# Kernel optimization log

Hardware: AMD Instinct MI355X
Metric: run time of the kernel (lower is better)

## Reference

```python
import jax, jax.numpy as jnp
import numpy as np

H = W = 192
C = 256
MAX_FEATURES = 2048
NUM_UP = 4  # num_upsampling scaling steps: pos -> pos*2 + 0.5 each step

# HandcraftedLocalizationModule filters (D2-Net)
DI  = [[0., -0.5, 0.], [0., 0., 0.], [0., 0.5, 0.]]
DJ  = [[0., 0., 0.], [-0.5, 0., 0.5], [0., 0., 0.]]
DII = [[0., 1., 0.], [0., -2., 0.], [0., 1., 0.]]
DJJ = [[0., 0., 0.], [1., -2., 1.], [0., 0., 0.]]
DIJ = [[0.25, 0., -0.25], [0., 0., 0.], [-0.25, 0., 0.25]]


def _conv3(x, k):
    # x: [H,W]; 3x3 cross-correlation, padding 1 (matches F.conv2d)
    k = jnp.asarray(k, x.dtype)
    return jax.lax.conv_general_dilated(x[None, None], k[None, None],
                                        window_strides=(1, 1),
                                        padding=[(1, 1), (1, 1)])[0, 0]


def _process_scale(feat, score):
    # feat: [C,H,W] dense descriptors, score: [H,W] attention/detection map
    Hm, Wm = score.shape
    # --- NMS: 3x3 maxpool, keep only local maxima (x[lmax != x] = 0) ---
    lmax = jax.lax.reduce_window(score, -jnp.inf, jax.lax.max,
                                 (3, 3), (1, 1), [(1, 1), (1, 1)])
    det = jnp.where(lmax == score, score, 0.0)
    valid = det != 0.0  # torch.nonzero equivalent (fixed-shape mask)
    # --- handcrafted localization (2x2 Newton step on the raw score map) ---
    di, dj = _conv3(score, DI), _conv3(score, DJ)
    dii, djj, dij = _conv3(score, DII), _conv3(score, DJJ), _conv3(score, DIJ)
    dd = dii * djj - dij * dij
    dd = jnp.where(dd == 0.0, 1e-20, dd)  # degenerate Hessian -> huge step, rejected by |.|<0.5
    step_i = -(djj * di - dij * dj) / dd
    step_j = -(-dij * di + dii * dj) / dd
    valid &= (jnp.abs(step_i) < 0.5) & (jnp.abs(step_j) < 0.5)
    ii, jj = jnp.meshgrid(jnp.arange(Hm, dtype=score.dtype),
                          jnp.arange(Wm, dtype=score.dtype), indexing='ij')
    ki = jnp.where(valid, ii + step_i, 0.0)
    kj = jnp.where(valid, jj + step_j, 0.0)
    # --- bilinear interpolation of dense features at sub-pixel keypoints ---
    i0 = jnp.floor(ki)
    j0 = jnp.floor(kj)
    valid &= (i0 >= 0) & (j0 >= 0) & (i0 + 1 <= Hm - 1) & (j0 + 1 <= Wm - 1)
    i0c = jnp.clip(i0, 0, Hm - 2).astype(jnp.int32)
    j0c = jnp.clip(j0, 0, Wm - 2).astype(jnp.int32)
    wi = ki - i0c
    wj = kj - j0c
    desc = (feat[:, i0c, j0c] * (1 - wi) * (1 - wj)
            + feat[:, i0c, j0c + 1] * (1 - wi) * wj
            + feat[:, i0c + 1, j0c] * wi * (1 - wj)
            + feat[:, i0c + 1, j0c + 1] * wi * wj)  # [C,H,W]
    norm = jnp.maximum(jnp.sqrt(jnp.sum(desc * desc, axis=0)), 1e-12)
    desc = desc / norm  # F.normalize(dim=0)
    # --- upscale positions: pos = pos*2 + 0.5 repeated NUM_UP times ---
    for _ in range(NUM_UP):
        ki = ki * 2 + 0.5
        kj = kj * 2 + 0.5
    scores = jnp.where(valid, det, -jnp.inf)  # invalid padded with -inf
    kp = jnp.stack([kj, ki], axis=-1).reshape(-1, 2)  # [:, [1,0]] swap -> (x, y)
    return kp, desc.reshape(desc.shape[0], -1).T, scores.reshape(-1), det


def setup_inputs() -> dict:
    key = jax.random.key(0)
    ks = jax.random.split(key, 6)
    return {
        "feat_early": jax.random.normal(ks[0], (1, C, H, W), jnp.float32),
        "feat_middle": jax.random.normal(ks[1], (1, C, H, W), jnp.float32),
        "feat_deep": jax.random.normal(ks[2], (1, C, H, W), jnp.float32),
        "score_early": jax.random.uniform(ks[3], (1, 1, H, W), jnp.float32),
        "score_middle": jax.random.uniform(ks[4], (1, 1, H, W), jnp.float32),
        "score_deep": jax.random.uniform(ks[5], (1, 1, H, W), jnp.float32),
    }


def reference(feat_early, feat_middle, feat_deep, score_early, score_middle, score_deep):
    feats = [feat_early[0], feat_middle[0], feat_deep[0]]
    smaps = [score_early[0, 0], score_middle[0, 0], score_deep[0, 0]]
    kps, descs, scs, dets = zip(*[_process_scale(f, s) for f, s in zip(feats, smaps)])
    kp = jnp.concatenate(kps)      # [3HW, 2]
    desc = jnp.concatenate(descs)  # [3HW, C]
    sc = jnp.concatenate(scs)      # [3HW]
    # torch.sort(descending) + thresh/max_features cap == top_k over padded scores
    top_s, idx = jax.lax.top_k(sc, MAX_FEATURES)
    sel = jnp.isfinite(top_s)
    keypoints = jnp.where(sel[:, None], kp[idx], 0.0)
    descriptors = jnp.where(sel[:, None], desc[idx], 0.0)
    scores = jnp.where(sel, top_s, 0.0)
    return keypoints, descriptors, scores, dets[0], dets[1], dets[2]
```

## Files before the change

### kernel.cpp

```cpp
#include <hip/hip_runtime.h>

#pragma clang fp contract(off)

#define H_ 192
#define W_ 192
#define HW_ (192 * 192)
#define NSC 3
#define NCAND (NSC * HW_)
#define CCH 256
#define KMAX 2048
#define NBIN 4096

#define KP_OFF 0
#define DESC_OFF (KMAX * 2)
#define SC_OFF (DESC_OFF + KMAX * CCH)
#define DET_OFF (SC_OFF + KMAX)

typedef unsigned long long u64;
typedef unsigned int u32;

#define CNT_OFF 884736
#define SLOT_OFF 884800
#define GH_OFF 917568
#define SARR_OFF 933952
#define CUR_OFF 950400
#define SURV_OFF 966784

__device__ __forceinline__ u32 key_bin(u32 sb) {
    if (sb >= 0xBF800000u) return NBIN - 1;
    if (sb >= 0xBF000000u) return 2048u + ((sb >> 12) & 0x7FFu);
    return (sb >> 20) & 0x7FFu;
}

__device__ __forceinline__ void newton_pixel(const float* __restrict__ sm, int i, int j,
                                             float& det, float& ki, float& kj, bool& valid) {
    float v[3][3];
#pragma unroll
    for (int a = 0; a < 3; ++a) {
#pragma unroll
        for (int b = 0; b < 3; ++b) {
            int ii = i + a - 1, jj = j + b - 1;
            bool in = (ii >= 0) && (ii < H_) && (jj >= 0) && (jj < W_);
            v[a][b] = in ? sm[ii * W_ + jj] : 0.0f;
        }
    }
    float c = v[1][1];
    float mx = v[0][0];
    mx = fmaxf(mx, v[0][1]); mx = fmaxf(mx, v[0][2]);
    mx = fmaxf(mx, v[1][0]); mx = fmaxf(mx, c);
    mx = fmaxf(mx, v[1][2]); mx = fmaxf(mx, v[2][0]);
    mx = fmaxf(mx, v[2][1]); mx = fmaxf(mx, v[2][2]);
    det = (mx == c) ? c : 0.0f;
    float di  = -0.5f * v[0][1] + 0.5f * v[2][1];
    float dj  = -0.5f * v[1][0] + 0.5f * v[1][2];
    float dii = v[0][1] - 2.0f * c + v[2][1];
    float djj = v[1][0] - 2.0f * c + v[1][2];
    float dij = 0.25f * v[0][0] - 0.25f * v[0][2] - 0.25f * v[2][0] + 0.25f * v[2][2];
    float dd = dii * djj - dij * dij;
    if (dd == 0.0f) dd = 1e-20f;
    float step_i = -(djj * di - dij * dj) / dd;
    float step_j = -(-dij * di + dii * dj) / dd;
    valid = (det != 0.0f) && (fabsf(step_i) < 0.5f) && (fabsf(step_j) < 0.5f);
    ki = valid ? ((float)i + step_i) : 0.0f;
    kj = valid ? ((float)j + step_j) : 0.0f;
    float i0 = floorf(ki), j0 = floorf(kj);
    valid = valid && (i0 >= 0.0f) && (j0 >= 0.0f) &&
            (i0 + 1.0f <= (float)(H_ - 1)) && (j0 + 1.0f <= (float)(W_ - 1));
}

__device__ __forceinline__ void decode_gid(u32 gid, int& s, int& i, int& j) {
    s = (int)(gid / HW_);
    int rem = (int)gid - s * HW_;
    i = rem / W_;
    j = rem - i * W_;
}

__global__ __launch_bounds__(256) void cand_kernel(
    const float* __restrict__ s0, const float* __restrict__ s1, const float* __restrict__ s2,
    float* __restrict__ out, u64* __restrict__ fin, u32* __restrict__ cnts,
    u32* __restrict__ ghist) {
    __shared__ u32 lcnt, base;
    int tid = threadIdx.x;
    if (tid == 0) lcnt = 0;
    __syncthreads();
    int t = blockIdx.x * 256 + tid;
    bool valid = false;
    u64 key = 0;
    {
        int s, i, j;
        decode_gid((u32)t, s, i, j);
        const float* sm = (s == 0) ? s0 : (s == 1) ? s1 : s2;
        float det, ki, kj;
        newton_pixel(sm, i, j, det, ki, kj, valid);
        out[DET_OFF + t] = det;
        if (valid) {
            u32 sb = __float_as_uint(det) | 0x80000000u;
            key = ((u64)sb << 32) | (u64)(0xFFFFFFFFu - (u32)t);
            atomicAdd(&ghist[key_bin(sb)], 1u);
        }
    }
    u32 lpos = 0;
    if (valid) lpos = atomicAdd(&lcnt, 1u);
    __syncthreads();
    if (tid == 0 && lcnt > 0) base = atomicAdd(&cnts[0], lcnt);
    __syncthreads();
    if (valid) fin[base + lpos] = key;
}

__global__ __launch_bounds__(256) void scan_kernel(
    const u32* __restrict__ ghist, u32* __restrict__ sarr, u32* __restrict__ cursor,
    u32* __restrict__ cnts) {
    __shared__ u32 ls[NBIN + 1];
    __shared__ u32 lT[256];
    int t = threadIdx.x;
    u32 chunk[16];
    u32 acc = 0;
#pragma unroll
    for (int k = 15; k >= 0; --k) {
        acc += ghist[t * 16 + k];
        chunk[k] = acc;
    }
    lT[t] = acc;
    __syncthreads();
    for (int off = 1; off < 256; off <<= 1) {
        u32 v = lT[t] + ((t + off < 256) ? lT[t + off] : 0u);
        __syncthreads();
        lT[t] = v;
        __syncthreads();
    }
    u32 add = (t < 255) ? lT[t + 1] : 0u;
#pragma unroll
    for (int k = 0; k < 16; ++k) ls[t * 16 + k] = chunk[k] + add;
    if (t == 0) ls[NBIN] = 0;
    __syncthreads();
#pragma unroll
    for (int k = 0; k < 16; ++k) {
        u32 b = t * 16 + k;
        sarr[b] = ls[b];
        cursor[b] = ls[b + 1];
        if (ls[b + 1] < KMAX && (b == 0 || ls[b] >= KMAX)) cnts[2] = ls[b];
    }
    if (t == 0) sarr[NBIN] = 0;
}

__global__ __launch_bounds__(256) void scatter_kernel(
    const u64* __restrict__ fin, const u32* __restrict__ sarr, u32* __restrict__ cursor,
    u32* __restrict__ cnts, u64* __restrict__ surv) {
    u32 n = cnts[0];
    for (u32 idx = blockIdx.x * 256 + threadIdx.x; idx < n; idx += 64 * 256) {
        u64 key = fin[idx];
        u32 b = key_bin((u32)(key >> 32));
        if (sarr[b + 1] < KMAX) {
            u32 pos = atomicAdd(&cursor[b], 1u);
            surv[pos] = key;
        }
    }
}

__global__ __launch_bounds__(256) void rank_kernel(
    const u64* __restrict__ surv, const u32* __restrict__ sarr, const u32* __restrict__ cnts,
    const float* __restrict__ s0, const float* __restrict__ s1, const float* __restrict__ s2,
    float4* __restrict__ slot) {
    u32 m = cnts[2];
    for (u32 p = blockIdx.x * 256 + threadIdx.x; p < m; p += 32 * 256) {
        u64 key = surv[p];
        u32 b = key_bin((u32)(key >> 32));
        u32 lo = sarr[b + 1], hi = sarr[b];
        u32 rank = lo;
        for (u32 q = lo; q < hi; ++q) rank += (surv[q] > key) ? 1u : 0u;
        if (rank < KMAX) {
            u32 gid = 0xFFFFFFFFu - (u32)(key & 0xFFFFFFFFull);
            int s, i, j;
            decode_gid(gid, s, i, j);
            const float* sm = (s == 0) ? s0 : (s == 1) ? s1 : s2;
            float det, ki, kj;
            bool valid;
            newton_pixel(sm, i, j, det, ki, kj, valid);
            slot[rank] = make_float4(ki, kj, det, (float)s);
        }
    }
}

__global__ __launch_bounds__(256) void output_kernel(
    const float4* __restrict__ slot,
    const float* __restrict__ f0, const float* __restrict__ f1, const float* __restrict__ f2,
    float* __restrict__ out) {
    __shared__ float red[4];
    int r = blockIdx.x;
    int tid = threadIdx.x;
    float4 info = slot[r];
    if (info.z == 0.0f) {
        out[DESC_OFF + r * CCH + tid] = 0.0f;
        if (tid == 0) {
            out[SC_OFF + r] = 0.0f;
            out[KP_OFF + r * 2 + 0] = 0.0f;
            out[KP_OFF + r * 2 + 1] = 0.0f;
        }
        return;
    }
    float ki = info.x, kj = info.y;
    int s = (int)info.w;
    const float* feat = (s == 0) ? f0 : (s == 1) ? f1 : f2;
    int i0 = (int)floorf(ki), j0 = (int)floorf(kj);
    float wi = ki - (float)i0;
    float wj = kj - (float)j0;
    const float* p = feat + (size_t)tid * HW_ + i0 * W_ + j0;
    float f00 = p[0], f01 = p[1], f10 = p[W_], f11 = p[W_ + 1];
    float d = f00 * (1.0f - wi) * (1.0f - wj) + f01 * (1.0f - wi) * wj +
              f10 * wi * (1.0f - wj) + f11 * wi * wj;
    float sq = d * d;
#pragma unroll
    for (int o = 32; o > 0; o >>= 1) sq += __shfl_down(sq, o, 64);
    if ((tid & 63) == 0) red[tid >> 6] = sq;
    __syncthreads();
    float norm = fmaxf(sqrtf(red[0] + red[1] + red[2] + red[3]), 1e-12f);
    out[DESC_OFF + r * CCH + tid] = d / norm;
    if (tid == 0) {
        out[SC_OFF + r] = info.z;
        float x = kj, y = ki;
#pragma unroll
        for (int u = 0; u < 4; ++u) { x = x * 2.0f + 0.5f; y = y * 2.0f + 0.5f; }
        out[KP_OFF + r * 2 + 0] = x;
        out[KP_OFF + r * 2 + 1] = y;
    }
}

extern "C" void kernel_launch(void* const* d_in, const int* in_sizes, int n_in,
                              void* d_out, int out_size, void* d_ws, size_t ws_size,
                              hipStream_t stream) {
    const float* f0 = (const float*)d_in[0];
    const float* f1 = (const float*)d_in[1];
    const float* f2 = (const float*)d_in[2];
    const float* s0 = (const float*)d_in[3];
    const float* s1 = (const float*)d_in[4];
    const float* s2 = (const float*)d_in[5];
    float* out = (float*)d_out;

    char* ws = (char*)d_ws;
    u64* fin = (u64*)ws;
    u32* cnts = (u32*)(ws + CNT_OFF);
    float4* slot = (float4*)(ws + SLOT_OFF);
    u32* ghist = (u32*)(ws + GH_OFF);
    u32* sarr = (u32*)(ws + SARR_OFF);
    u32* cursor = (u32*)(ws + CUR_OFF);
    u64* surv = (u64*)(ws + SURV_OFF);

    hipMemsetAsync(ws + CNT_OFF, 0, 64 + KMAX * 16 + NBIN * 4, stream);
    cand_kernel<<<NCAND / 256, 256, 0, stream>>>(s0, s1, s2, out, fin, cnts, ghist);
    scan_kernel<<<1, 256, 0, stream>>>(ghist, sarr, cursor, cnts);
    scatter_kernel<<<64, 256, 0, stream>>>(fin, sarr, cursor, cnts, surv);
    rank_kernel<<<32, 256, 0, stream>>>(surv, sarr, cnts, s0, s1, s2, slot);
    output_kernel<<<KMAX, 256, 0, stream>>>(slot, f0, f1, f2, out);
}
```

Measured before the change: 165.3 us.

## Fuse pipeline stages via last-block-done counters and use wave-per-keypoint output

After: 227.3 us. +37.5%, slower.

```diff
diff --git a/kernel.cpp b/kernel.cpp
--- a/kernel.cpp
+++ b/kernel.cpp
@@ -10,6 +10,8 @@
 #define CCH 256
 #define KMAX 2048
 #define NBIN 4096
+#define NBLK_CAND (NCAND / 256)
+#define NBLK_SCAT 64
 
 #define KP_OFF 0
 #define DESC_OFF (KMAX * 2)
@@ -75,27 +77,29 @@
     j = rem - i * W_;
 }
 
-__global__ __launch_bounds__(256) void cand_kernel(
+__global__ __launch_bounds__(256) void cand_scan_kernel(
     const float* __restrict__ s0, const float* __restrict__ s1, const float* __restrict__ s2,
     float* __restrict__ out, u64* __restrict__ fin, u32* __restrict__ cnts,
-    u32* __restrict__ ghist) {
-    __shared__ u32 lcnt, base;
+    u32* __restrict__ ghist, u32* __restrict__ sarr, u32* __restrict__ cursor) {
+    __shared__ u32 lcnt, base, go;
+    __shared__ u32 ls[NBIN + 1];
+    __shared__ u32 lT[256];
     int tid = threadIdx.x;
     if (tid == 0) lcnt = 0;
     __syncthreads();
-    int t = blockIdx.x * 256 + tid;
+    int g = blockIdx.x * 256 + tid;
     bool valid = false;
     u64 key = 0;
     {
         int s, i, j;
-        decode_gid((u32)t, s, i, j);
+        decode_gid((u32)g, s, i, j);
         const float* sm = (s == 0) ? s0 : (s == 1) ? s1 : s2;
         float det, ki, kj;
         newton_pixel(sm, i, j, det, ki, kj, valid);
-        out[DET_OFF + t] = det;
+        out[DET_OFF + g] = det;
         if (valid) {
             u32 sb = __float_as_uint(det) | 0x80000000u;
-            key = ((u64)sb << 32) | (u64)(0xFFFFFFFFu - (u32)t);
+            key = ((u64)sb << 32) | (u64)(0xFFFFFFFFu - (u32)g);
             atomicAdd(&ghist[key_bin(sb)], 1u);
         }
     }
@@ -105,49 +109,52 @@
     if (tid == 0 && lcnt > 0) base = atomicAdd(&cnts[0], lcnt);
     __syncthreads();
     if (valid) fin[base + lpos] = key;
-}
-
-__global__ __launch_bounds__(256) void scan_kernel(
-    const u32* __restrict__ ghist, u32* __restrict__ sarr, u32* __restrict__ cursor,
-    u32* __restrict__ cnts) {
-    __shared__ u32 ls[NBIN + 1];
-    __shared__ u32 lT[256];
-    int t = threadIdx.x;
+
+    __threadfence();
+    __syncthreads();
+    if (tid == 0) go = (atomicAdd(&cnts[1], 1u) == NBLK_CAND - 1) ? 1u : 0u;
+    __syncthreads();
+    if (go == 0) return;
+    __threadfence();
+
     u32 chunk[16];
     u32 acc = 0;
 #pragma unroll
     for (int k = 15; k >= 0; --k) {
-        acc += ghist[t * 16 + k];
+        acc += ghist[tid * 16 + k];
         chunk[k] = acc;
     }
-    lT[t] = acc;
+    lT[tid] = acc;
     __syncthreads();
     for (int off = 1; off < 256; off <<= 1) {
-        u32 v = lT[t] + ((t + off < 256) ? lT[t + off] : 0u);
+        u32 v = lT[tid] + ((tid + off < 256) ? lT[tid + off] : 0u);
         __syncthreads();
-        lT[t] = v;
+        lT[tid] = v;
         __syncthreads();
     }
-    u32 add = (t < 255) ? lT[t + 1] : 0u;
-#pragma unroll
-    for (int k = 0; k < 16; ++k) ls[t * 16 + k] = chunk[k] + add;
-    if (t == 0) ls[NBIN] = 0;
+    u32 add = (tid < 255) ? lT[tid + 1] : 0u;
+#pragma unroll
+    for (int k = 0; k < 16; ++k) ls[tid * 16 + k] = chunk[k] + add;
+    if (tid == 0) ls[NBIN] = 0;
     __syncthreads();
 #pragma unroll
     for (int k = 0; k < 16; ++k) {
-        u32 b = t * 16 + k;
+        u32 b = tid * 16 + k;
         sarr[b] = ls[b];
         cursor[b] = ls[b + 1];
         if (ls[b + 1] < KMAX && (b == 0 || ls[b] >= KMAX)) cnts[2] = ls[b];
     }
-    if (t == 0) sarr[NBIN] = 0;
-}
-
-__global__ __launch_bounds__(256) void scatter_kernel(
+    if (tid == 0) sarr[NBIN] = 0;
+}
+
+__global__ __launch_bounds__(256) void scatter_rank_kernel(
     const u64* __restrict__ fin, const u32* __restrict__ sarr, u32* __restrict__ cursor,
-    u32* __restrict__ cnts, u64* __restrict__ surv) {
+    u32* __restrict__ cnts, u64* __restrict__ surv,
+    const float* __restrict__ s0, const float* __restrict__ s1, const float* __restrict__ s2,
+    float4* __restrict__ slot) {
+    __shared__ u32 go;
     u32 n = cnts[0];
-    for (u32 idx = blockIdx.x * 256 + threadIdx.x; idx < n; idx += 64 * 256) {
+    for (u32 idx = blockIdx.x * 256 + threadIdx.x; idx < n; idx += NBLK_SCAT * 256) {
         u64 key = fin[idx];
         u32 b = key_bin((u32)(key >> 32));
         if (sarr[b + 1] < KMAX) {
@@ -155,14 +162,15 @@
             surv[pos] = key;
         }
     }
-}
-
-__global__ __launch_bounds__(256) void rank_kernel(
-    const u64* __restrict__ surv, const u32* __restrict__ sarr, const u32* __restrict__ cnts,
-    const float* __restrict__ s0, const float* __restrict__ s1, const float* __restrict__ s2,
-    float4* __restrict__ slot) {
+    __threadfence();
+    __syncthreads();
+    if (threadIdx.x == 0) go = (atomicAdd(&cnts[3], 1u) == NBLK_SCAT - 1) ? 1u : 0u;
+    __syncthreads();
+    if (go == 0) return;
+    __threadfence();
+
     u32 m = cnts[2];
-    for (u32 p = blockIdx.x * 256 + threadIdx.x; p < m; p += 32 * 256) {
+    for (u32 p = threadIdx.x; p < m; p += 256) {
         u64 key = surv[p];
         u32 b = key_bin((u32)(key >> 32));
         u32 lo = sarr[b + 1], hi = sarr[b];
@@ -185,43 +193,40 @@
     const float4* __restrict__ slot,
     const float* __restrict__ f0, const float* __restrict__ f1, const float* __restrict__ f2,
     float* __restrict__ out) {
-    __shared__ float red[4];
-    int r = blockIdx.x;
-    int tid = threadIdx.x;
+    int lane = threadIdx.x & 63;
+    int r = blockIdx.x * 4 + (threadIdx.x >> 6);
     float4 info = slot[r];
-    if (info.z == 0.0f) {
-        out[DESC_OFF + r * CCH + tid] = 0.0f;
-        if (tid == 0) {
-            out[SC_OFF + r] = 0.0f;
-            out[KP_OFF + r * 2 + 0] = 0.0f;
-            out[KP_OFF + r * 2 + 1] = 0.0f;
-        }
-        return;
-    }
+    bool pad = (info.z == 0.0f);
     float ki = info.x, kj = info.y;
     int s = (int)info.w;
     const float* feat = (s == 0) ? f0 : (s == 1) ? f1 : f2;
     int i0 = (int)floorf(ki), j0 = (int)floorf(kj);
     float wi = ki - (float)i0;
     float wj = kj - (float)j0;
-    const float* p = feat + (size_t)tid * HW_ + i0 * W_ + j0;
-    float f00 = p[0], f01 = p[1], f10 = p[W_], f11 = p[W_ + 1];
-    float d = f00 * (1.0f - wi) * (1.0f - wj) + f01 * (1.0f - wi) * wj +
-              f10 * wi * (1.0f - wj) + f11 * wi * wj;
-    float sq = d * d;
-#pragma unroll
-    for (int o = 32; o > 0; o >>= 1) sq += __shfl_down(sq, o, 64);
-    if ((tid & 63) == 0) red[tid >> 6] = sq;
-    __syncthreads();
-    float norm = fmaxf(sqrtf(red[0] + red[1] + red[2] + red[3]), 1e-12f);
-    out[DESC_OFF + r * CCH + tid] = d / norm;
-    if (tid == 0) {
-        out[SC_OFF + r] = info.z;
+    const float* p = feat + (size_t)lane * HW_ + i0 * W_ + j0;
+    float d[4];
+    float sq = 0.0f;
+#pragma unroll
+    for (int k = 0; k < 4; ++k) {
+        const float* q = p + (size_t)k * 64 * HW_;
+        float f00 = q[0], f01 = q[1], f10 = q[W_], f11 = q[W_ + 1];
+        d[k] = f00 * (1.0f - wi) * (1.0f - wj) + f01 * (1.0f - wi) * wj +
+               f10 * wi * (1.0f - wj) + f11 * wi * wj;
+        sq += d[k] * d[k];
+    }
+#pragma unroll
+    for (int o = 1; o < 64; o <<= 1) sq += __shfl_xor(sq, o, 64);
+    float norm = fmaxf(sqrtf(sq), 1e-12f);
+#pragma unroll
+    for (int k = 0; k < 4; ++k)
+        out[DESC_OFF + r * CCH + k * 64 + lane] = pad ? 0.0f : d[k] / norm;
+    if (lane == 0) {
         float x = kj, y = ki;
 #pragma unroll
         for (int u = 0; u < 4; ++u) { x = x * 2.0f + 0.5f; y = y * 2.0f + 0.5f; }
-        out[KP_OFF + r * 2 + 0] = x;
-        out[KP_OFF + r * 2 + 1] = y;
+        out[SC_OFF + r] = pad ? 0.0f : info.z;
+        out[KP_OFF + r * 2 + 0] = pad ? 0.0f : x;
+        out[KP_OFF + r * 2 + 1] = pad ? 0.0f : y;
     }
 }
 
@@ -246,9 +251,9 @@
     u64* surv = (u64*)(ws + SURV_OFF);
 
     hipMemsetAsync(ws + CNT_OFF, 0, 64 + KMAX * 16 + NBIN * 4, stream);
-    cand_kernel<<<NCAND / 256, 256, 0, stream>>>(s0, s1, s2, out, fin, cnts, ghist);
-    scan_kernel<<<1, 256, 0, stream>>>(ghist, sarr, cursor, cnts);
-    scatter_kernel<<<64, 256, 0, stream>>>(fin, sarr, cursor, cnts, surv);
-    rank_kernel<<<32, 256, 0, stream>>>(surv, sarr, cnts, s0, s1, s2, slot);
-    output_kernel<<<KMAX, 256, 0, stream>>>(slot, f0, f1, f2, out);
-}
+    cand_scan_kernel<<<NBLK_CAND, 256, 0, stream>>>(s0, s1, s2, out, fin, cnts, ghist,
+                                                    sarr, cursor);
+    scatter_rank_kernel<<<NBLK_SCAT, 256, 0, stream>>>(fin, sarr, cursor, cnts, surv,
+                                                       s0, s1, s2, slot);
+    output_kernel<<<KMAX / 4, 256, 0, stream>>>(slot, f0, f1, f2, out);
+}
```
